# Optimization experiments

Measured on AMD Instinct MI355X. Metric: run time of the kernel, lower is better.

The kernel has to match this reference:

```python
import jax, jax.numpy as jnp
import numpy as np

EMBD_SIZE = 128
NUM_HEADS = 8
HEAD_SIZE = 16

def setup_inputs() -> dict:
    key = jax.random.key(0)
    ks = jax.random.split(key, 6)
    B, S = 8, 2048
    x = jax.random.normal(ks[0], (B, S, EMBD_SIZE), dtype=jnp.float32)
    # per-head Linear weights, torch layout [out, in] stacked over heads -> [H, hs, E]
    sc = 1.0 / np.sqrt(EMBD_SIZE)
    Wk = jax.random.normal(ks[1], (NUM_HEADS, HEAD_SIZE, EMBD_SIZE), dtype=jnp.float32) * sc
    Wq = jax.random.normal(ks[2], (NUM_HEADS, HEAD_SIZE, EMBD_SIZE), dtype=jnp.float32) * sc
    Wv = jax.random.normal(ks[3], (NUM_HEADS, HEAD_SIZE, EMBD_SIZE), dtype=jnp.float32) * sc
    Wp = jax.random.normal(ks[4], (EMBD_SIZE, NUM_HEADS * HEAD_SIZE), dtype=jnp.float32) * sc
    bp = jax.random.normal(ks[5], (EMBD_SIZE,), dtype=jnp.float32) * 0.01
    return {"x": x, "Wk": Wk, "Wq": Wq, "Wv": Wv, "Wp": Wp, "bp": bp}

def reference(x, Wk, Wq, Wv, Wp, bp):
    # x: [B,S,E]; W{k,q,v}: [H,hs,E]; Wp: [E,H*hs]
    B, S, E = x.shape
    H, hs, _ = Wk.shape
    q = jnp.einsum('bse,hde->bhsd', x, Wq)
    k = jnp.einsum('bse,hde->bhsd', x, Wk)
    v = jnp.einsum('bse,hde->bhsd', x, Wv)
    # NOTE: original code MULTIPLIES by sqrt(head_size) (k.shape[-1]**0.5)
    scores = jnp.einsum('bhsd,bhtd->bhst', q, k) * (hs ** 0.5)
    wei = jax.nn.softmax(scores, axis=-1)  # dropout is identity in eval mode
    out = jnp.einsum('bhst,bhtd->bhsd', wei, v)
    # concat heads along last dim: [B,S,H*hs]
    out = out.transpose(0, 2, 1, 3).reshape(B, S, H * hs)
    return out @ Wp.T + bp
```

## Files before the change

### kernel.cpp

```cpp
#include <hip/hip_runtime.h>
#include <hip/hip_bf16.h>

constexpr int Bb  = 8;
constexpr int Ss  = 2048;
constexpr int Ee  = 128;
constexpr int Hh  = 8;
constexpr int HSs = 16;
constexpr int QKVSZ = Bb * Hh * Ss * HSs;

typedef _Float16 f16;
typedef __attribute__((ext_vector_type(8)))  _Float16 f16x8;
typedef __attribute__((ext_vector_type(16))) float f32x16;

constexpr float QSCALE = 5.770780163555854f;

__device__ __forceinline__ unsigned pack_rtz(float lo, float hi) {
    union { __fp16 __attribute__((ext_vector_type(2))) h; unsigned u; } c;
    c.h = __builtin_amdgcn_cvt_pkrtz(lo, hi);
    return c.u;
}
__device__ __forceinline__ unsigned pack_rne(float lo, float hi) {
    union { __attribute__((ext_vector_type(2))) _Float16 h; unsigned u; } c;
    c.h[0] = (f16)lo; c.h[1] = (f16)hi;
    return c.u;
}

__global__ __launch_bounds__(256) void prep_x(const float* __restrict__ x,
                                              f16* __restrict__ xh) {
    int i = (blockIdx.x * 256 + threadIdx.x) * 4;
    float4 v = *(const float4*)(x + i);
    union { f16 h[4]; uint2 u; } c;
    c.h[0] = (f16)v.x; c.h[1] = (f16)v.y; c.h[2] = (f16)v.z; c.h[3] = (f16)v.w;
    *(uint2*)(xh + i) = c.u;
}
__global__ __launch_bounds__(256) void prep_w(
    const float* __restrict__ Wq, const float* __restrict__ Wk,
    const float* __restrict__ Wv, const float* __restrict__ Wp,
    f16* __restrict__ wh)
{
    int i = (blockIdx.x * 256 + threadIdx.x) * 4;
    const float* src = (i < 16384) ? (Wq + i)
                     : (i < 32768) ? (Wk + i - 16384)
                     : (i < 49152) ? (Wv + i - 32768) : (Wp + i - 49152);
    float4 v = *(const float4*)src;
    union { f16 h[4]; uint2 u; } c;
    c.h[0] = (f16)v.x; c.h[1] = (f16)v.y; c.h[2] = (f16)v.z; c.h[3] = (f16)v.w;
    *(uint2*)(wh + i) = c.u;
}

__global__ __launch_bounds__(256) void qkv_kernel(
    const f16* __restrict__ xh, const f16* __restrict__ wh,
    f16* __restrict__ qo, f16* __restrict__ ko, f16* __restrict__ vo)
{
    const int mat  = blockIdx.y;
    const f16* W   = wh + mat * 16384;
    const int wv_  = threadIdx.x >> 6, lane = threadIdx.x & 63;
    const int h    = lane >> 5, n31 = lane & 31;
    const int rowbase = blockIdx.x * 128 + wv_ * 32;

    const f16* xr = xh + (size_t)(rowbase + n31) * Ee + 8 * h;
    f16x8 A[8];
#pragma unroll
    for (int t = 0; t < 8; ++t) A[t] = *(const f16x8*)(xr + 16 * t);

    f16* dst = (mat == 0) ? qo : ((mat == 1) ? ko : vo);
    const float scale = (mat == 1) ? QSCALE : 1.f;

#pragma unroll
    for (int g = 0; g < 4; ++g) {
        const int c = g * 32 + n31;
        const f16* wr = W + (size_t)c * Ee + 8 * h;
        f32x16 acc = {};
#pragma unroll
        for (int t = 0; t < 8; ++t)
            acc = __builtin_amdgcn_mfma_f32_32x32x16_f16(A[t], *(const f16x8*)(wr + 16 * t), acc, 0, 0, 0);

        const int head = c >> 4, d = c & 15;
#pragma unroll
        for (int r = 0; r < 16; ++r) {
            const int R = rowbase + (r & 3) + 8 * (r >> 2) + 4 * h;
            const int b = R >> 11, s = R & 2047;
            const int bh = b * Hh + head;
            f16 val = (f16)(acc[r] * scale);
            if (mat == 2) {
                dst[(size_t)bh * 32768 + (s >> 6) * 1024 + ((s >> 4) & 3) * 256
                    + ((s >> 3) & 1) * 128 + d * 8 + (s & 7)] = val;
            } else {
                dst[((size_t)bh * Ss + s) * HSs + d] = val;
            }
        }
    }
}

__device__ __forceinline__ void cb_exchange(const unsigned* pw, int h,
                                            f16x8& Blo, f16x8& Bhi) {
    unsigned exa = (unsigned)__shfl_xor((int)(h ? pw[0] : pw[2]), 32, 64);
    unsigned exb = (unsigned)__shfl_xor((int)(h ? pw[1] : pw[3]), 32, 64);
    unsigned exc = (unsigned)__shfl_xor((int)(h ? pw[4] : pw[6]), 32, 64);
    unsigned exd = (unsigned)__shfl_xor((int)(h ? pw[5] : pw[7]), 32, 64);
    union { unsigned u[4]; f16x8 v; } B1, B2;
    if (h == 0) {
        B1.u[0] = pw[0]; B1.u[1] = pw[1]; B1.u[2] = exa; B1.u[3] = exb;
        B2.u[0] = pw[4]; B2.u[1] = pw[5]; B2.u[2] = exc; B2.u[3] = exd;
    } else {
        B1.u[0] = exa; B1.u[1] = exb; B1.u[2] = pw[2]; B1.u[3] = pw[3];
        B2.u[0] = exc; B2.u[1] = exd; B2.u[2] = pw[6]; B2.u[3] = pw[7];
    }
    Blo = B1.v; Bhi = B2.v;
}

__global__ __launch_bounds__(256) void attn_kernel(
    const f16* __restrict__ qg, const f16* __restrict__ kg,
    const f16* __restrict__ vg, f16* __restrict__ og)
{
    __shared__ __align__(16) f16 Ks[64 * 24];
    __shared__ __align__(16) f16 Vf[4 * 64 * 8];

    const int blk  = blockIdx.x;
    const int w_   = blk >> 3;
    const int bh   = (blk & 7) * 8 + (w_ >> 4);
    const int qblk = w_ & 15;
    const int wv_  = threadIdx.x >> 6;
    const int lane = threadIdx.x & 63;
    const int h    = lane >> 5;
    const int q31  = lane & 31;
    const int qbase = qblk * 128 + wv_ * 32;

    {
        const int i = threadIdx.x & 127;
        if (threadIdx.x < 128)
            *(uint4*)&Vf[((i >> 5) * 512 + ((i >> 4) & 1) * 256 + 128 + (i & 15) * 8)] = (uint4){0,0,0,0};
    }

    const f16x8 qf = *(const f16x8*)(qg + ((size_t)bh * Ss + qbase + q31) * HSs + 8 * h);

    const bool isK = threadIdx.x < 128;
    const int  i   = threadIdx.x & 127;
    const f16* gsrc = isK ? (kg + ((size_t)bh * Ss) * HSs + i * 8)
                          : (vg + (size_t)bh * 32768 + i * 8);
    f16* ldst = isK ? &Ks[(i >> 1) * 24 + (i & 1) * 8]
                    : &Vf[(i >> 5) * 512 + ((i >> 4) & 1) * 256 + (i & 15) * 8];
    f16x8 sreg = *(const f16x8*)gsrc;

    f32x16 acc = {};
    const f32x16 z16 = {};
    float m = -1e30f, l = 0.f;

    for (int it = 0; it < Ss / 64; ++it) {
        __syncthreads();
        *(f16x8*)ldst = sreg;
        __syncthreads();
        if (it < Ss / 64 - 1) { gsrc += 1024; sreg = *(const f16x8*)gsrc; }

        f16x8 ka0 = *(const f16x8*)&Ks[q31 * 24 + 8 * h];
        f16x8 ka1 = *(const f16x8*)&Ks[(32 + q31) * 24 + 8 * h];
        f32x16 st0 = __builtin_amdgcn_mfma_f32_32x32x16_f16(ka0, qf, z16, 0, 0, 0);
        f32x16 st1 = __builtin_amdgcn_mfma_f32_32x32x16_f16(ka1, qf, z16, 0, 0, 0);

        float mx = st0[0];
#pragma unroll
        for (int t = 1; t < 16; ++t) mx = fmaxf(mx, st0[t]);
#pragma unroll
        for (int t = 0; t < 16; ++t) mx = fmaxf(mx, st1[t]);
        mx = fmaxf(mx, __shfl_xor(mx, 32, 64));
        const float mnew = fmaxf(m, mx);
        const float corr = __builtin_amdgcn_exp2f(m - mnew);
        float p0[16], p1[16];
        float rs = 0.f;
#pragma unroll
        for (int t = 0; t < 16; ++t) { p0[t] = __builtin_amdgcn_exp2f(st0[t] - mnew); rs += p0[t]; }
#pragma unroll
        for (int t = 0; t < 16; ++t) { p1[t] = __builtin_amdgcn_exp2f(st1[t] - mnew); rs += p1[t]; }
        rs += __shfl_xor(rs, 32, 64);
        l = l * corr + rs;
#pragma unroll
        for (int r = 0; r < 8; ++r) acc[r] *= corr;
        m = mnew;

        unsigned pw0[8], pw1[8];
#pragma unroll
        for (int r = 0; r < 8; ++r) pw0[r] = pack_rtz(p0[2 * r], p0[2 * r + 1]);
#pragma unroll
        for (int r = 0; r < 8; ++r) pw1[r] = pack_rtz(p1[2 * r], p1[2 * r + 1]);
        f16x8 B1, B2, B3, B4;
        cb_exchange(pw0, h, B1, B2);
        cb_exchange(pw1, h, B3, B4);

        f16x8 va0 = *(const f16x8*)&Vf[0 * 512 + lane * 8];
        f16x8 va1 = *(const f16x8*)&Vf[1 * 512 + lane * 8];
        f16x8 va2 = *(const f16x8*)&Vf[2 * 512 + lane * 8];
        f16x8 va3 = *(const f16x8*)&Vf[3 * 512 + lane * 8];
        acc = __builtin_amdgcn_mfma_f32_32x32x16_f16(va0, B1, acc, 0, 0, 0);
        acc = __builtin_amdgcn_mfma_f32_32x32x16_f16(va1, B2, acc, 0, 0, 0);
        acc = __builtin_amdgcn_mfma_f32_32x32x16_f16(va2, B3, acc, 0, 0, 0);
        acc = __builtin_amdgcn_mfma_f32_32x32x16_f16(va3, B4, acc, 0, 0, 0);
    }

    const float inv = 1.f / l;
    const int b = bh >> 3, head = bh & 7;
    f16* op = og + ((size_t)b * Ss + qbase + q31) * Ee + head * HSs;
    uint2 lo = { pack_rne(acc[0] * inv, acc[1] * inv), pack_rne(acc[2] * inv, acc[3] * inv) };
    uint2 hi = { pack_rne(acc[4] * inv, acc[5] * inv), pack_rne(acc[6] * inv, acc[7] * inv) };
    *(uint2*)(op + 4 * h)     = lo;
    *(uint2*)(op + 8 + 4 * h) = hi;
}

__global__ __launch_bounds__(256) void proj_kernel(
    const f16* __restrict__ oh, const f16* __restrict__ wph,
    const float* __restrict__ bp, float* __restrict__ out)
{
    const int wv_ = threadIdx.x >> 6, lane = threadIdx.x & 63;
    const int h = lane >> 5, n31 = lane & 31;
    const int rowbase = blockIdx.x * 128 + wv_ * 32;

    const f16* ar = oh + (size_t)(rowbase + n31) * Ee + 8 * h;
    f16x8 A[8];
#pragma unroll
    for (int t = 0; t < 8; ++t) A[t] = *(const f16x8*)(ar + 16 * t);

#pragma unroll
    for (int g = 0; g < 2; ++g) {
        const int e = blockIdx.y * 64 + g * 32 + n31;
        const f16* wr = wph + (size_t)e * Ee + 8 * h;
        f32x16 acc = {};
#pragma unroll
        for (int t = 0; t < 8; ++t)
            acc = __builtin_amdgcn_mfma_f32_32x32x16_f16(A[t], *(const f16x8*)(wr + 16 * t), acc, 0, 0, 0);
        const float bias = bp[e];
#pragma unroll
        for (int r = 0; r < 16; ++r) {
            const int R = rowbase + (r & 3) + 8 * (r >> 2) + 4 * h;
            out[(size_t)R * Ee + e] = acc[r] + bias;
        }
    }
}

extern "C" void kernel_launch(void* const* d_in, const int* in_sizes, int n_in,
                              void* d_out, int out_size, void* d_ws, size_t ws_size,
                              hipStream_t stream)
{
    const float* x  = (const float*)d_in[0];
    const float* Wk = (const float*)d_in[1];
    const float* Wq = (const float*)d_in[2];
    const float* Wv = (const float*)d_in[3];
    const float* Wp = (const float*)d_in[4];
    const float* bp = (const float*)d_in[5];
    float* out = (float*)d_out;

    f16* ws = (f16*)d_ws;
    f16* xh = ws;
    f16* qh = ws + (size_t)QKVSZ;
    f16* kh = ws + (size_t)2 * QKVSZ;
    f16* vh = ws + (size_t)3 * QKVSZ;
    f16* oh = ws + (size_t)4 * QKVSZ;
    f16* wh = ws + (size_t)5 * QKVSZ;

    prep_x<<<QKVSZ / 1024, 256, 0, stream>>>(x, xh);
    prep_w<<<64, 256, 0, stream>>>(Wq, Wk, Wv, Wp, wh);
    qkv_kernel<<<dim3(Bb * Ss / 128, 3), 256, 0, stream>>>(xh, wh, qh, kh, vh);
    attn_kernel<<<Bb * Hh * (Ss / 128), 256, 0, stream>>>(qh, kh, vh, oh);
    proj_kernel<<<dim3(Bb * Ss / 128, 2), 256, 0, stream>>>(oh, wh + 49152, bp, out);
}
```

Measured before the change: 158.1 us.

## Fuse fp32-to-fp16 conversion into GEMMs and double-buffer attention K/V tiles

Removes the separate prep_x and prep_w conversion kernels. The QKV and projection kernels now read fp32 x and weights directly, converting x through a padded shared-memory tile and weights in registers. Attention K/V shared tiles are double-buffered so each iteration needs one barrier instead of two. The projection kernel now uses 128-thread blocks over 64-row tiles covering all 128 outputs. The trade-off is that fp32 weights are reloaded and reconverted by every block, and the qkv kernel reads x in fp32 three times, once per matrix.

```diff
diff --git a/kernel.cpp b/kernel.cpp
--- a/kernel.cpp
+++ b/kernel.cpp
@@ -24,44 +24,44 @@
     c.h[0] = (f16)lo; c.h[1] = (f16)hi;
     return c.u;
 }
-
-__global__ __launch_bounds__(256) void prep_x(const float* __restrict__ x,
-                                              f16* __restrict__ xh) {
-    int i = (blockIdx.x * 256 + threadIdx.x) * 4;
-    float4 v = *(const float4*)(x + i);
-    union { f16 h[4]; uint2 u; } c;
-    c.h[0] = (f16)v.x; c.h[1] = (f16)v.y; c.h[2] = (f16)v.z; c.h[3] = (f16)v.w;
-    *(uint2*)(xh + i) = c.u;
-}
-__global__ __launch_bounds__(256) void prep_w(
-    const float* __restrict__ Wq, const float* __restrict__ Wk,
-    const float* __restrict__ Wv, const float* __restrict__ Wp,
-    f16* __restrict__ wh)
-{
-    int i = (blockIdx.x * 256 + threadIdx.x) * 4;
-    const float* src = (i < 16384) ? (Wq + i)
-                     : (i < 32768) ? (Wk + i - 16384)
-                     : (i < 49152) ? (Wv + i - 32768) : (Wp + i - 49152);
-    float4 v = *(const float4*)src;
-    union { f16 h[4]; uint2 u; } c;
-    c.h[0] = (f16)v.x; c.h[1] = (f16)v.y; c.h[2] = (f16)v.z; c.h[3] = (f16)v.w;
-    *(uint2*)(wh + i) = c.u;
+__device__ __forceinline__ f16x8 cvt8(const float* p) {
+    float4 a = *(const float4*)p;
+    float4 b = *(const float4*)(p + 4);
+    f16x8 r;
+    r[0] = (f16)a.x; r[1] = (f16)a.y; r[2] = (f16)a.z; r[3] = (f16)a.w;
+    r[4] = (f16)b.x; r[5] = (f16)b.y; r[6] = (f16)b.z; r[7] = (f16)b.w;
+    return r;
 }
 
 __global__ __launch_bounds__(256) void qkv_kernel(
-    const f16* __restrict__ xh, const f16* __restrict__ wh,
+    const float* __restrict__ x,  const float* __restrict__ Wq,
+    const float* __restrict__ Wk, const float* __restrict__ Wv,
     f16* __restrict__ qo, f16* __restrict__ ko, f16* __restrict__ vo)
 {
-    const int mat  = blockIdx.y;
-    const f16* W   = wh + mat * 16384;
-    const int wv_  = threadIdx.x >> 6, lane = threadIdx.x & 63;
-    const int h    = lane >> 5, n31 = lane & 31;
-    const int rowbase = blockIdx.x * 128 + wv_ * 32;
-
-    const f16* xr = xh + (size_t)(rowbase + n31) * Ee + 8 * h;
+    constexpr int LDW = 136;
+    __shared__ __align__(16) f16 Xs[128 * LDW];
+
+    const int mat = blockIdx.y;
+    const float* W = (mat == 0) ? Wq : ((mat == 1) ? Wk : Wv);
+    const int rowbase = blockIdx.x * 128;
+
+    for (int idx = threadIdx.x; idx < 128 * 32; idx += 256) {
+        const int r = idx >> 5, cp = idx & 31;
+        float4 v = *(const float4*)(x + (size_t)(rowbase + r) * Ee + cp * 4);
+        union { f16 h[4]; uint2 u; } c;
+        c.h[0] = (f16)v.x; c.h[1] = (f16)v.y; c.h[2] = (f16)v.z; c.h[3] = (f16)v.w;
+        *(uint2*)&Xs[r * LDW + cp * 4] = c.u;
+    }
+    __syncthreads();
+
+    const int wv_ = threadIdx.x >> 6, lane = threadIdx.x & 63;
+    const int h = lane >> 5, n31 = lane & 31;
+    const int rb2 = rowbase + wv_ * 32;
+
     f16x8 A[8];
 #pragma unroll
-    for (int t = 0; t < 8; ++t) A[t] = *(const f16x8*)(xr + 16 * t);
+    for (int t = 0; t < 8; ++t)
+        A[t] = *(const f16x8*)&Xs[(wv_ * 32 + n31) * LDW + 16 * t + 8 * h];
 
     f16* dst = (mat == 0) ? qo : ((mat == 1) ? ko : vo);
     const float scale = (mat == 1) ? QSCALE : 1.f;
@@ -69,16 +69,16 @@
 #pragma unroll
     for (int g = 0; g < 4; ++g) {
         const int c = g * 32 + n31;
-        const f16* wr = W + (size_t)c * Ee + 8 * h;
+        const float* wr = W + (size_t)c * Ee + 8 * h;
         f32x16 acc = {};
 #pragma unroll
         for (int t = 0; t < 8; ++t)
-            acc = __builtin_amdgcn_mfma_f32_32x32x16_f16(A[t], *(const f16x8*)(wr + 16 * t), acc, 0, 0, 0);
+            acc = __builtin_amdgcn_mfma_f32_32x32x16_f16(A[t], cvt8(wr + 16 * t), acc, 0, 0, 0);
 
         const int head = c >> 4, d = c & 15;
 #pragma unroll
         for (int r = 0; r < 16; ++r) {
-            const int R = rowbase + (r & 3) + 8 * (r >> 2) + 4 * h;
+            const int R = rb2 + (r & 3) + 8 * (r >> 2) + 4 * h;
             const int b = R >> 11, s = R & 2047;
             const int bh = b * Hh + head;
             f16 val = (f16)(acc[r] * scale);
@@ -113,8 +113,8 @@
     const f16* __restrict__ qg, const f16* __restrict__ kg,
     const f16* __restrict__ vg, f16* __restrict__ og)
 {
-    __shared__ __align__(16) f16 Ks[64 * 24];
-    __shared__ __align__(16) f16 Vf[4 * 64 * 8];
+    __shared__ __align__(16) f16 Ks[2][64 * 24];
+    __shared__ __align__(16) f16 Vf[2][2048];
 
     const int blk  = blockIdx.x;
     const int w_   = blk >> 3;
@@ -127,20 +127,24 @@
     const int qbase = qblk * 128 + wv_ * 32;
 
     {
-        const int i = threadIdx.x & 127;
-        if (threadIdx.x < 128)
-            *(uint4*)&Vf[((i >> 5) * 512 + ((i >> 4) & 1) * 256 + 128 + (i & 15) * 8)] = (uint4){0,0,0,0};
+        const int i = threadIdx.x;
+        const int b = i >> 7, rem = i & 127;
+        const int g = rem >> 5, hh = (rem >> 4) & 1, sub = i & 15;
+        *(uint4*)&Vf[b][g * 512 + hh * 256 + 128 + sub * 8] = (uint4){0, 0, 0, 0};
     }
 
     const f16x8 qf = *(const f16x8*)(qg + ((size_t)bh * Ss + qbase + q31) * HSs + 8 * h);
 
     const bool isK = threadIdx.x < 128;
     const int  i   = threadIdx.x & 127;
-    const f16* gsrc = isK ? (kg + ((size_t)bh * Ss) * HSs + i * 8)
+    const f16* gsrc = isK ? (kg + (size_t)bh * Ss * HSs + i * 8)
                           : (vg + (size_t)bh * 32768 + i * 8);
-    f16* ldst = isK ? &Ks[(i >> 1) * 24 + (i & 1) * 8]
-                    : &Vf[(i >> 5) * 512 + ((i >> 4) & 1) * 256 + (i & 15) * 8];
+    const int koff = (i >> 1) * 24 + (i & 1) * 8;
+    const int voff = (i >> 5) * 512 + ((i >> 4) & 1) * 256 + (i & 15) * 8;
     f16x8 sreg = *(const f16x8*)gsrc;
+
+    if (isK) *(f16x8*)&Ks[0][koff] = sreg; else *(f16x8*)&Vf[0][voff] = sreg;
+    gsrc += 1024; sreg = *(const f16x8*)gsrc;
 
     f32x16 acc = {};
     const f32x16 z16 = {};
@@ -148,12 +152,15 @@
 
     for (int it = 0; it < Ss / 64; ++it) {
         __syncthreads();
-        *(f16x8*)ldst = sreg;
-        __syncthreads();
-        if (it < Ss / 64 - 1) { gsrc += 1024; sreg = *(const f16x8*)gsrc; }
-
-        f16x8 ka0 = *(const f16x8*)&Ks[q31 * 24 + 8 * h];
-        f16x8 ka1 = *(const f16x8*)&Ks[(32 + q31) * 24 + 8 * h];
+        if (it < Ss / 64 - 1) {
+            const int nb = (it + 1) & 1;
+            if (isK) *(f16x8*)&Ks[nb][koff] = sreg; else *(f16x8*)&Vf[nb][voff] = sreg;
+            gsrc += 1024; sreg = *(const f16x8*)gsrc;
+        }
+        const int cb = it & 1;
+
+        f16x8 ka0 = *(const f16x8*)&Ks[cb][q31 * 24 + 8 * h];
+        f16x8 ka1 = *(const f16x8*)&Ks[cb][(32 + q31) * 24 + 8 * h];
         f32x16 st0 = __builtin_amdgcn_mfma_f32_32x32x16_f16(ka0, qf, z16, 0, 0, 0);
         f32x16 st1 = __builtin_amdgcn_mfma_f32_32x32x16_f16(ka1, qf, z16, 0, 0, 0);
 
@@ -186,10 +193,10 @@
         cb_exchange(pw0, h, B1, B2);
         cb_exchange(pw1, h, B3, B4);
 
-        f16x8 va0 = *(const f16x8*)&Vf[0 * 512 + lane * 8];
-        f16x8 va1 = *(const f16x8*)&Vf[1 * 512 + lane * 8];
-        f16x8 va2 = *(const f16x8*)&Vf[2 * 512 + lane * 8];
-        f16x8 va3 = *(const f16x8*)&Vf[3 * 512 + lane * 8];
+        f16x8 va0 = *(const f16x8*)&Vf[cb][0 * 512 + lane * 8];
+        f16x8 va1 = *(const f16x8*)&Vf[cb][1 * 512 + lane * 8];
+        f16x8 va2 = *(const f16x8*)&Vf[cb][2 * 512 + lane * 8];
+        f16x8 va3 = *(const f16x8*)&Vf[cb][3 * 512 + lane * 8];
         acc = __builtin_amdgcn_mfma_f32_32x32x16_f16(va0, B1, acc, 0, 0, 0);
         acc = __builtin_amdgcn_mfma_f32_32x32x16_f16(va1, B2, acc, 0, 0, 0);
         acc = __builtin_amdgcn_mfma_f32_32x32x16_f16(va2, B3, acc, 0, 0, 0);
@@ -205,31 +212,42 @@
     *(uint2*)(op + 8 + 4 * h) = hi;
 }
 
-__global__ __launch_bounds__(256) void proj_kernel(
-    const f16* __restrict__ oh, const f16* __restrict__ wph,
+__global__ __launch_bounds__(128) void proj_kernel(
+    const f16* __restrict__ oh, const float* __restrict__ Wp,
     const float* __restrict__ bp, float* __restrict__ out)
 {
+    constexpr int LDW = 136;
+    __shared__ __align__(16) f16 Os[64 * LDW];
+    const int rowbase = blockIdx.x * 64;
+
+    for (int idx = threadIdx.x; idx < 64 * 16; idx += 128) {
+        const int r = idx >> 4, cp = idx & 15;
+        *(f16x8*)&Os[r * LDW + cp * 8] =
+            *(const f16x8*)(oh + (size_t)(rowbase + r) * Ee + cp * 8);
+    }
+    __syncthreads();
+
     const int wv_ = threadIdx.x >> 6, lane = threadIdx.x & 63;
     const int h = lane >> 5, n31 = lane & 31;
-    const int rowbase = blockIdx.x * 128 + wv_ * 32;
-
-    const f16* ar = oh + (size_t)(rowbase + n31) * Ee + 8 * h;
+    const int rb2 = rowbase + wv_ * 32;
+
     f16x8 A[8];
 #pragma unroll
-    for (int t = 0; t < 8; ++t) A[t] = *(const f16x8*)(ar + 16 * t);
-
-#pragma unroll
-    for (int g = 0; g < 2; ++g) {
-        const int e = blockIdx.y * 64 + g * 32 + n31;
-        const f16* wr = wph + (size_t)e * Ee + 8 * h;
+    for (int t = 0; t < 8; ++t)
+        A[t] = *(const f16x8*)&Os[(wv_ * 32 + n31) * LDW + 16 * t + 8 * h];
+
+#pragma unroll
+    for (int g = 0; g < 4; ++g) {
+        const int e = g * 32 + n31;
+        const float* wr = Wp + (size_t)e * Ee + 8 * h;
         f32x16 acc = {};
 #pragma unroll
         for (int t = 0; t < 8; ++t)
-            acc = __builtin_amdgcn_mfma_f32_32x32x16_f16(A[t], *(const f16x8*)(wr + 16 * t), acc, 0, 0, 0);
+            acc = __builtin_amdgcn_mfma_f32_32x32x16_f16(A[t], cvt8(wr + 16 * t), acc, 0, 0, 0);
         const float bias = bp[e];
 #pragma unroll
         for (int r = 0; r < 16; ++r) {
-            const int R = rowbase + (r & 3) + 8 * (r >> 2) + 4 * h;
+            const int R = rb2 + (r & 3) + 8 * (r >> 2) + 4 * h;
             out[(size_t)R * Ee + e] = acc[r] + bias;
         }
     }
@@ -248,16 +266,12 @@
     float* out = (float*)d_out;
 
     f16* ws = (f16*)d_ws;
-    f16* xh = ws;
-    f16* qh = ws + (size_t)QKVSZ;
-    f16* kh = ws + (size_t)2 * QKVSZ;
-    f16* vh = ws + (size_t)3 * QKVSZ;
-    f16* oh = ws + (size_t)4 * QKVSZ;
-    f16* wh = ws + (size_t)5 * QKVSZ;
-
-    prep_x<<<QKVSZ / 1024, 256, 0, stream>>>(x, xh);
-    prep_w<<<64, 256, 0, stream>>>(Wq, Wk, Wv, Wp, wh);
-    qkv_kernel<<<dim3(Bb * Ss / 128, 3), 256, 0, stream>>>(xh, wh, qh, kh, vh);
+    f16* qh = ws;
+    f16* kh = ws + (size_t)QKVSZ;
+    f16* vh = ws + (size_t)2 * QKVSZ;
+    f16* oh = ws + (size_t)3 * QKVSZ;
+
+    qkv_kernel<<<dim3(Bb * Ss / 128, 3), 256, 0, stream>>>(x, Wq, Wk, Wv, qh, kh, vh);
     attn_kernel<<<Bb * Hh * (Ss / 128), 256, 0, stream>>>(qh, kh, vh, oh);
-    proj_kernel<<<dim3(Bb * Ss / 128, 2), 256, 0, stream>>>(oh, wh + 49152, bp, out);
-}
+    proj_kernel<<<Bb * Ss / 64, 128, 0, stream>>>(oh, Wp, bp, out);
+}
```

Result: slower. 171.2 us (+8.3%).
